# Kernel optimization log

Measured on AMD Instinct MI355X. Metric: run time of the kernel, lower is better.

## Reference

```python
import jax, jax.numpy as jnp
import numpy as np

EMBED_DIM = 1024
NUM_HEADS = 16
HEAD_DIM = EMBED_DIM // NUM_HEADS
SEQ_LEN = 2048
B = 2


def setup_inputs() -> dict:
    key = jax.random.key(0)
    ks = jax.random.split(key, 6)
    x = jax.random.normal(ks[0], (B, SEQ_LEN, EMBED_DIM), dtype=jnp.float32)
    # Linear params (torch Linear: y = x @ W.T + b); store W as [in, out] for einsum
    qkv_w = jax.random.normal(ks[1], (EMBED_DIM, 3 * EMBED_DIM), dtype=jnp.float32) * (EMBED_DIM ** -0.5)
    qkv_b = jnp.zeros((3 * EMBED_DIM,), dtype=jnp.float32)
    proj_w = jax.random.normal(ks[2], (EMBED_DIM, EMBED_DIM), dtype=jnp.float32) * (EMBED_DIM ** -0.5)
    proj_b = jnp.zeros((EMBED_DIM,), dtype=jnp.float32)
    # relative position bias table [2L-1, H], trunc_normal std=0.02 ~ normal*0.02
    bias_table = jax.random.normal(ks[3], (2 * SEQ_LEN - 1, NUM_HEADS), dtype=jnp.float32) * 0.02
    return {"x": x, "qkv_w": qkv_w, "qkv_b": qkv_b, "proj_w": proj_w, "proj_b": proj_b, "bias_table": bias_table}


def _rel_pos_index(L):
    coords = jnp.arange(L)
    return (coords[None, :] - coords[:, None]) + (SEQ_LEN - 1)  # [L, L] int


def reference(x, qkv_w, qkv_b, proj_w, proj_b, bias_table):
    Bsz, L, C = x.shape
    scale = HEAD_DIM ** -0.5
    qkv = x @ qkv_w + qkv_b                               # [B, L, 3C]
    qkv = qkv.reshape(Bsz, L, 3, NUM_HEADS, HEAD_DIM)
    q = jnp.transpose(qkv[:, :, 0], (0, 2, 1, 3))          # [B, H, L, D]
    k = jnp.transpose(qkv[:, :, 1], (0, 2, 1, 3))
    v = jnp.transpose(qkv[:, :, 2], (0, 2, 1, 3))
    attn = jnp.einsum('bhqd,bhkd->bhqk', q, k) * scale     # [B, H, L, L]
    rel_bias = bias_table[_rel_pos_index(L)]               # [L, L, H]
    attn = attn + jnp.transpose(rel_bias, (2, 0, 1))[None]  # broadcast over batch
    attn = jax.nn.softmax(attn, axis=-1)
    out = jnp.einsum('bhqk,bhkd->bhqd', attn, v)           # [B, H, L, D]
    out = jnp.transpose(out, (0, 2, 1, 3)).reshape(Bsz, L, C)
    return out @ proj_w + proj_b
```

## Files before the change

### kernel.cpp

```cpp
#include <hip/hip_runtime.h>

typedef short bf16x4 __attribute__((ext_vector_type(4)));
typedef short bf16x8 __attribute__((ext_vector_type(8)));
typedef float f32x4 __attribute__((ext_vector_type(4)));
typedef float f32x16 __attribute__((ext_vector_type(16)));

__device__ __forceinline__ unsigned short f2bf(float f) {
  union { float f; unsigned int u; } v; v.f = f;
  unsigned int r = v.u + 0x7FFFu + ((v.u >> 16) & 1u);
  return (unsigned short)(r >> 16);
}

__device__ __forceinline__ float exp2_fast(float x) {
  float r;
  asm("v_exp_f32 %0, %1" : "=v"(r) : "v"(x));
  return r;
}

__device__ __forceinline__ unsigned int cvt_pk_bf16(float lo, float hi) {
  unsigned int r;
  asm("v_cvt_pk_bf16_f32 %0, %1, %2" : "=v"(r) : "v"(lo), "v"(hi));
  return r;
}

__device__ __forceinline__ void gld_lds16(const void* g, void* l) {
  __builtin_amdgcn_global_load_lds(
      (const __attribute__((address_space(1))) unsigned int*)g,
      (__attribute__((address_space(3))) unsigned int*)l, 16, 0, 0);
}


__global__ __launch_bounds__(256) void k_convert_x(const float4* __restrict__ in,
                                                   ushort4* __restrict__ out) {
  int id = blockIdx.x * 256 + threadIdx.x;
  float4 v = in[id];
  ushort4 o;
  o.x = f2bf(v.x); o.y = f2bf(v.y); o.z = f2bf(v.z); o.w = f2bf(v.w);
  out[id] = o;
}

__global__ __launch_bounds__(256) void k_transpose_bf16(const float* __restrict__ in,
                                                        unsigned short* __restrict__ out,
                                                        int R, int C) {
  __shared__ float tile[32][33];
  int tx = threadIdx.x, ty = threadIdx.y;
  int c0 = blockIdx.x * 32, r0 = blockIdx.y * 32;
#pragma unroll
  for (int i = 0; i < 32; i += 8) tile[ty + i][tx] = in[(size_t)(r0 + ty + i) * C + c0 + tx];
  __syncthreads();
#pragma unroll
  for (int i = 0; i < 32; i += 8) out[(size_t)(c0 + ty + i) * R + r0 + tx] = f2bf(tile[tx][ty + i]);
}

__global__ __launch_bounds__(256) void k_bias_cols(const float* __restrict__ bt,
                                                   float* __restrict__ bh) {
  int i = blockIdx.x * 256 + threadIdx.x;
  if (i < 4095 * 16) bh[(i & 15) * 4096 + (i >> 4)] = bt[i] * 1.44269504089f;
}

template <int EPI>
__global__ __launch_bounds__(256) void k_gemm(const unsigned short* __restrict__ A,
                                              const unsigned short* __restrict__ Bt,
                                              const float* __restrict__ bias,
                                              float* __restrict__ Cf,
                                              unsigned short* __restrict__ qb,
                                              unsigned short* __restrict__ kb,
                                              unsigned short* __restrict__ vtb) {
  __shared__ unsigned short Alds[128 * 64];
  __shared__ unsigned short Blds[128 * 64];
  const int t = threadIdx.x;
  const int l = t & 63, w = t >> 6;
  const int l15 = l & 15, l4 = l >> 4;
  const int wm = w >> 1, wn = w & 1;

  constexpr int NX = EPI ? 24 : 8;
  constexpr int NWG = EPI ? 768 : 256;
  const int hwid = blockIdx.x + NX * blockIdx.y;
  const int swz = (hwid & 7) * (NWG >> 3) + (hwid >> 3);
  const int bn = (swz % NX) * 128;
  const int bm = (swz / NX) * 128;

  const int srow = t >> 3;
  const int scl = (t & 7) ^ (srow & 7);
  const unsigned short* ag = A + (size_t)(bm + srow) * 1024 + scl * 8;
  const unsigned short* bg = Bt + (size_t)(bn + srow) * 1024 + scl * 8;

  f32x4 acc[4][4];
#pragma unroll
  for (int i = 0; i < 4; ++i)
#pragma unroll
    for (int j = 0; j < 4; ++j) acc[i][j] = (f32x4){0.f, 0.f, 0.f, 0.f};

  for (int kt = 0; kt < 16; ++kt) {
#pragma unroll
    for (int q = 0; q < 4; ++q) {
      gld_lds16(ag + (size_t)q * 32 * 1024 + kt * 64, &Alds[(q * 256 + t) * 8]);
      gld_lds16(bg + (size_t)q * 32 * 1024 + kt * 64, &Blds[(q * 256 + t) * 8]);
    }
    __syncthreads();
#pragma unroll
    for (int kc = 0; kc < 2; ++kc) {
      bf16x8 af[4], bv[4];
#pragma unroll
      for (int i = 0; i < 4; ++i) {
        int ra = wm * 64 + i * 16 + l15;
        af[i] = *(const bf16x8*)&Alds[ra * 64 + (((kc * 4 + l4) ^ (l15 & 7))) * 8];
        int rb = wn * 64 + i * 16 + l15;
        bv[i] = *(const bf16x8*)&Blds[rb * 64 + (((kc * 4 + l4) ^ (l15 & 7))) * 8];
      }
#pragma unroll
      for (int i = 0; i < 4; ++i)
#pragma unroll
        for (int jn = 0; jn < 4; ++jn)
          acc[i][jn] = __builtin_amdgcn_mfma_f32_16x16x32_bf16(af[i], bv[jn], acc[i][jn], 0, 0, 0);
    }
    __syncthreads();
  }

#pragma unroll
  for (int i = 0; i < 4; ++i) {
#pragma unroll
    for (int jn = 0; jn < 4; ++jn) {
      int n = bn + wn * 64 + jn * 16 + l15;
      float bval = bias[n];
#pragma unroll
      for (int j = 0; j < 4; ++j) {
        int m = bm + wm * 64 + i * 16 + l4 * 4 + j;
        float v = acc[i][jn][j] + bval;
        if (EPI == 0) {
          Cf[(size_t)m * 1024 + n] = v;
        } else {
          int which = n >> 10, hh = (n >> 6) & 15, d = n & 63;
          int bb = m >> 11, pos = m & 2047;
          int bhh = bb * 16 + hh;
          if (which == 0)
            qb[((size_t)bhh * 2048 + pos) * 64 + d] = f2bf(v * 0.18033688f);
          else if (which == 1)
            kb[((size_t)bhh * 2048 + pos) * 64 + d] = f2bf(v);
          else
            vtb[((size_t)bhh * 64 + d) * 2048 + pos] = f2bf(v);
        }
      }
    }
  }
}

__global__ __launch_bounds__(256) void k_attn(const unsigned short* __restrict__ qbuf,
                                              const unsigned short* __restrict__ kbuf,
                                              const unsigned short* __restrict__ vtbuf,
                                              const float* __restrict__ biash,
                                              unsigned short* __restrict__ aout) {
  __shared__ __align__(16) unsigned short Klds[2][64 * 64];
  __shared__ __align__(16) unsigned short Vlds[2][64 * 64];

  const int t = threadIdx.x;
  const int w = t >> 6, l = t & 63;
  const int l31 = l & 31, hi = l >> 5;

  const int bid = blockIdx.x;
  const int swzb = (bid & 7) * 64 + (bid >> 3);
  const int qt = swzb & 15;
  const int bh = swzb >> 4;
  const int h = bh & 15, b = bh >> 4;
  const int qbase = qt * 128;
  const int wq = qbase + w * 32;

  bf16x8 qB[4];
  {
    const unsigned short* qrow = qbuf + ((size_t)bh * 2048 + wq + l31) * 64;
#pragma unroll
    for (int ds = 0; ds < 4; ++ds) qB[ds] = *(const bf16x8*)&qrow[ds * 16 + hi * 8];
  }

  f32x16 O[2];
#pragma unroll
  for (int i = 0; i < 16; ++i) { O[0][i] = 0.f; O[1][i] = 0.f; }
  float m_run = -3e38f, l_run = 0.f;

  const int c0r = t >> 3, c0c = t & 7;
  const unsigned short* kg = kbuf + ((size_t)bh * 2048 + c0r) * 64 + c0c * 8;
  const unsigned short* vg = vtbuf + ((size_t)bh * 64 + c0r) * 2048 + c0c * 8;
  const int wKV = c0r * 64 + ((c0c ^ (c0r & 7)) * 8);

  {
    bf16x8 k0 = *(const bf16x8*)(kg);
    bf16x8 k1 = *(const bf16x8*)(kg + 32 * 64);
    bf16x8 v0 = *(const bf16x8*)(vg);
    bf16x8 v1 = *(const bf16x8*)(vg + 32 * 2048);
    *(bf16x8*)&Klds[0][wKV] = k0;
    *(bf16x8*)&Klds[0][wKV + 2048] = k1;
    *(bf16x8*)&Vlds[0][wKV] = v0;
    *(bf16x8*)&Vlds[0][wKV + 2048] = v1;
  }
  __syncthreads();

  const float* bgl = biash + h * 4096 + 2047 - (wq + l31) + 4 * hi;

  for (int kt = 0; kt < 32; ++kt) {
    const int cur = kt & 1;

    bf16x8 kst0, kst1, vst0, vst1;
    if (kt < 31) {
      const unsigned short* kga = kg + (size_t)(kt + 1) * 4096;
      const unsigned short* vga = vg + (kt + 1) * 64;
      kst0 = *(const bf16x8*)(kga);
      kst1 = *(const bf16x8*)(kga + 32 * 64);
      vst0 = *(const bf16x8*)(vga);
      vst1 = *(const bf16x8*)(vga + 32 * 2048);
    }
    const int kbase = kt * 64;

    f32x4 bq[2][4];
#pragma unroll
    for (int kt2 = 0; kt2 < 2; ++kt2)
#pragma unroll
      for (int g = 0; g < 4; ++g)
        __builtin_memcpy(&bq[kt2][g], &bgl[kbase + 32 * kt2 + 8 * g], 16);

    f32x16 sacc[2];
#pragma unroll
    for (int i = 0; i < 16; ++i) { sacc[0][i] = 0.f; sacc[1][i] = 0.f; }
    __builtin_amdgcn_s_setprio(1);
#pragma unroll
    for (int kt2 = 0; kt2 < 2; ++kt2) {
      int row = kt2 * 32 + l31;
      int rsw = row & 7;
#pragma unroll
      for (int ds = 0; ds < 4; ++ds) {
        bf16x8 ka = *(const bf16x8*)&Klds[cur][row * 64 + (((2 * ds + hi) ^ rsw) * 8)];
        sacc[kt2] = __builtin_amdgcn_mfma_f32_32x32x16_bf16(ka, qB[ds], sacc[kt2], 0, 0, 0);
      }
    }
    __builtin_amdgcn_s_setprio(0);

#pragma unroll
    for (int kt2 = 0; kt2 < 2; ++kt2)
#pragma unroll
      for (int g = 0; g < 4; ++g)
#pragma unroll
        for (int r = 0; r < 4; ++r) sacc[kt2][4 * g + r] += bq[kt2][g][r];

    float mx;
    {
      float q0 = fmaxf(fmaxf(sacc[0][0], sacc[0][1]), fmaxf(sacc[0][2], sacc[0][3]));
      float q1 = fmaxf(fmaxf(sacc[0][4], sacc[0][5]), fmaxf(sacc[0][6], sacc[0][7]));
      float q2 = fmaxf(fmaxf(sacc[0][8], sacc[0][9]), fmaxf(sacc[0][10], sacc[0][11]));
      float q3 = fmaxf(fmaxf(sacc[0][12], sacc[0][13]), fmaxf(sacc[0][14], sacc[0][15]));
      float q4 = fmaxf(fmaxf(sacc[1][0], sacc[1][1]), fmaxf(sacc[1][2], sacc[1][3]));
      float q5 = fmaxf(fmaxf(sacc[1][4], sacc[1][5]), fmaxf(sacc[1][6], sacc[1][7]));
      float q6 = fmaxf(fmaxf(sacc[1][8], sacc[1][9]), fmaxf(sacc[1][10], sacc[1][11]));
      float q7 = fmaxf(fmaxf(sacc[1][12], sacc[1][13]), fmaxf(sacc[1][14], sacc[1][15]));
      mx = fmaxf(fmaxf(fmaxf(q0, q1), fmaxf(q2, q3)), fmaxf(fmaxf(q4, q5), fmaxf(q6, q7)));
      mx = fmaxf(mx, __shfl_xor(mx, 32));
    }

    if (__any(mx > m_run + 8.f)) {
      float mnew = fmaxf(m_run, mx);
      float alpha = exp2_fast(m_run - mnew);
      m_run = mnew;
      l_run *= alpha;
#pragma unroll
      for (int g = 0; g < 4; ++g)
#pragma unroll
        for (int r = 0; r < 4; ++r) {
          float a_lo = __shfl(alpha, 8 * g + r);
          float a_hi = __shfl(alpha, 8 * g + r + 4);
          float aq = hi ? a_hi : a_lo;
          O[0][4 * g + r] *= aq;
          O[1][4 * g + r] *= aq;
        }
    }

#pragma unroll
    for (int kt2 = 0; kt2 < 2; ++kt2)
#pragma unroll
      for (int i = 0; i < 16; ++i) sacc[kt2][i] = exp2_fast(sacc[kt2][i] - m_run);
    {
      float s0 = (sacc[0][0] + sacc[0][1]) + (sacc[0][2] + sacc[0][3]);
      float s1 = (sacc[0][4] + sacc[0][5]) + (sacc[0][6] + sacc[0][7]);
      float s2 = (sacc[0][8] + sacc[0][9]) + (sacc[0][10] + sacc[0][11]);
      float s3 = (sacc[0][12] + sacc[0][13]) + (sacc[0][14] + sacc[0][15]);
      float s4 = (sacc[1][0] + sacc[1][1]) + (sacc[1][2] + sacc[1][3]);
      float s5 = (sacc[1][4] + sacc[1][5]) + (sacc[1][6] + sacc[1][7]);
      float s6 = (sacc[1][8] + sacc[1][9]) + (sacc[1][10] + sacc[1][11]);
      float s7 = (sacc[1][12] + sacc[1][13]) + (sacc[1][14] + sacc[1][15]);
      float rs = ((s0 + s1) + (s2 + s3)) + ((s4 + s5) + (s6 + s7));
      rs += __shfl_xor(rs, 32);
      l_run += rs;
    }

    bf16x8 pa[2][2];
#pragma unroll
    for (int kt2 = 0; kt2 < 2; ++kt2)
#pragma unroll
      for (int mm = 0; mm < 2; ++mm) {
        union { unsigned int u[4]; bf16x8 v; } pk;
        pk.u[0] = cvt_pk_bf16(sacc[kt2][8 * mm + 0], sacc[kt2][8 * mm + 1]);
        pk.u[1] = cvt_pk_bf16(sacc[kt2][8 * mm + 2], sacc[kt2][8 * mm + 3]);
        pk.u[2] = cvt_pk_bf16(sacc[kt2][8 * mm + 4], sacc[kt2][8 * mm + 5]);
        pk.u[3] = cvt_pk_bf16(sacc[kt2][8 * mm + 6], sacc[kt2][8 * mm + 7]);
        pa[kt2][mm] = pk.v;
      }

    __builtin_amdgcn_s_setprio(1);
#pragma unroll
    for (int dt = 0; dt < 2; ++dt) {
      int row = dt * 32 + l31;
      int rsw = row & 7;
#pragma unroll
      for (int kt2 = 0; kt2 < 2; ++kt2)
#pragma unroll
        for (int mm = 0; mm < 2; ++mm) {
          int cA = (4 * kt2 + 2 * mm) ^ rsw;
          int cB = (4 * kt2 + 2 * mm + 1) ^ rsw;
          bf16x4 vlo = *(const bf16x4*)&Vlds[cur][row * 64 + cA * 8 + 4 * hi];
          bf16x4 vhi = *(const bf16x4*)&Vlds[cur][row * 64 + cB * 8 + 4 * hi];
          bf16x8 vb = __builtin_shufflevector(vlo, vhi, 0, 1, 2, 3, 4, 5, 6, 7);
          O[dt] = __builtin_amdgcn_mfma_f32_32x32x16_bf16(pa[kt2][mm], vb, O[dt], 0, 0, 0);
        }
    }
    __builtin_amdgcn_s_setprio(0);

    if (kt < 31) {
      *(bf16x8*)&Klds[cur ^ 1][wKV] = kst0;
      *(bf16x8*)&Klds[cur ^ 1][wKV + 2048] = kst1;
      *(bf16x8*)&Vlds[cur ^ 1][wKV] = vst0;
      *(bf16x8*)&Vlds[cur ^ 1][wKV + 2048] = vst1;
    }
    __syncthreads();
  }

  {
    float linv = 1.f / l_run;
#pragma unroll
    for (int g = 0; g < 4; ++g)
#pragma unroll
      for (int r = 0; r < 4; ++r) {
        float v_lo = __shfl(linv, 8 * g + r);
        float v_hi = __shfl(linv, 8 * g + r + 4);
        float sc = hi ? v_hi : v_lo;
        int q = wq + 8 * g + r + 4 * hi;
        size_t base = ((size_t)b * 2048 + q) * 1024 + h * 64 + l31;
        aout[base] = f2bf(O[0][4 * g + r] * sc);
        aout[base + 32] = f2bf(O[1][4 * g + r] * sc);
      }
  }
}


extern "C" void kernel_launch(void* const* d_in, const int* in_sizes, int n_in,
                              void* d_out, int out_size, void* d_ws, size_t ws_size,
                              hipStream_t stream) {
  const float* x = (const float*)d_in[0];
  const float* qkv_w = (const float*)d_in[1];
  const float* qkv_b = (const float*)d_in[2];
  const float* proj_w = (const float*)d_in[3];
  const float* proj_b = (const float*)d_in[4];
  const float* bias_table = (const float*)d_in[5];
  float* out = (float*)d_out;

  char* ws = (char*)d_ws;
  unsigned short* xb = (unsigned short*)(ws);
  unsigned short* wqkv = (unsigned short*)(ws + (size_t)(8u << 20));
  unsigned short* wproj = (unsigned short*)(ws + (size_t)(14u << 20));
  unsigned short* qb = (unsigned short*)(ws + (size_t)(16u << 20));
  unsigned short* kb = (unsigned short*)(ws + (size_t)(24u << 20));
  unsigned short* vtb = (unsigned short*)(ws + (size_t)(32u << 20));
  float* biash = (float*)(ws + (size_t)(40u << 20));

  unsigned short* attn_out = xb;

  k_convert_x<<<dim3(4096), dim3(256), 0, stream>>>((const float4*)x, (ushort4*)xb);
  k_transpose_bf16<<<dim3(96, 32), dim3(32, 8), 0, stream>>>(qkv_w, wqkv, 1024, 3072);
  k_transpose_bf16<<<dim3(32, 32), dim3(32, 8), 0, stream>>>(proj_w, wproj, 1024, 1024);
  k_bias_cols<<<dim3(256), dim3(256), 0, stream>>>(bias_table, biash);

  k_gemm<1><<<dim3(24, 32), dim3(256), 0, stream>>>(xb, wqkv, qkv_b, nullptr, qb, kb, vtb);
  k_attn<<<dim3(512), dim3(256), 0, stream>>>(qb, kb, vtb, biash, attn_out);
  k_gemm<0><<<dim3(8, 32), dim3(256), 0, stream>>>(attn_out, wproj, proj_b, out, nullptr, nullptr,
                                                   nullptr);
}
```

Before: 161.9 us.

## Double-buffer GEMM LDS with register-staged prefetch and XCD-aware tile mapping

The GEMM main loop moves from direct global-to-LDS loads with two barriers per k-step to a two-stage pipeline. Global loads for step k+2 go into registers while MFMAs run on the current LDS buffer, and the staged registers are written to the other LDS buffer, leaving one barrier per step. The block-to-tile mapping also changes to a 1D grid that groups each XCD's blocks into an 8x(12 or 4) tile region to improve L2 reuse. This costs double the LDS (64KB per block) and 16 extra VGPR vectors, which may lower occupancy.

```diff
diff --git a/kernel.cpp b/kernel.cpp
--- a/kernel.cpp
+++ b/kernel.cpp
@@ -21,12 +21,6 @@
   unsigned int r;
   asm("v_cvt_pk_bf16_f32 %0, %1, %2" : "=v"(r) : "v"(lo), "v"(hi));
   return r;
-}
-
-__device__ __forceinline__ void gld_lds16(const void* g, void* l) {
-  __builtin_amdgcn_global_load_lds(
-      (const __attribute__((address_space(1))) unsigned int*)g,
-      (__attribute__((address_space(3))) unsigned int*)l, 16, 0, 0);
 }
 
 
@@ -66,24 +60,23 @@
                                               unsigned short* __restrict__ qb,
                                               unsigned short* __restrict__ kb,
                                               unsigned short* __restrict__ vtb) {
-  __shared__ unsigned short Alds[128 * 64];
-  __shared__ unsigned short Blds[128 * 64];
+  __shared__ unsigned short Alds[2][128 * 64];
+  __shared__ unsigned short Blds[2][128 * 64];
   const int t = threadIdx.x;
   const int l = t & 63, w = t >> 6;
   const int l15 = l & 15, l4 = l >> 4;
   const int wm = w >> 1, wn = w & 1;
 
-  constexpr int NX = EPI ? 24 : 8;
-  constexpr int NWG = EPI ? 768 : 256;
-  const int hwid = blockIdx.x + NX * blockIdx.y;
-  const int swz = (hwid & 7) * (NWG >> 3) + (hwid >> 3);
-  const int bn = (swz % NX) * 128;
-  const int bm = (swz / NX) * 128;
+  const int hwid = blockIdx.x;
+  const int x = hwid & 7, loc = hwid >> 3;
+  const int bm = ((x >> 1) * 8 + (loc & 7)) * 128;
+  const int bn = ((x & 1) * (EPI ? 12 : 4) + (loc >> 3)) * 128;
 
   const int srow = t >> 3;
-  const int scl = (t & 7) ^ (srow & 7);
-  const unsigned short* ag = A + (size_t)(bm + srow) * 1024 + scl * 8;
-  const unsigned short* bg = Bt + (size_t)(bn + srow) * 1024 + scl * 8;
+  const int sc = t & 7;
+  const unsigned short* agl = A + (size_t)(bm + srow) * 1024 + sc * 8;
+  const unsigned short* bgl = Bt + (size_t)(bn + srow) * 1024 + sc * 8;
+  const int wls = srow * 64 + ((sc ^ (srow & 7)) * 8);
 
   f32x4 acc[4][4];
 #pragma unroll
@@ -91,31 +84,59 @@
 #pragma unroll
     for (int j = 0; j < 4; ++j) acc[i][j] = (f32x4){0.f, 0.f, 0.f, 0.f};
 
-  for (int kt = 0; kt < 16; ++kt) {
-#pragma unroll
-    for (int q = 0; q < 4; ++q) {
-      gld_lds16(ag + (size_t)q * 32 * 1024 + kt * 64, &Alds[(q * 256 + t) * 8]);
-      gld_lds16(bg + (size_t)q * 32 * 1024 + kt * 64, &Blds[(q * 256 + t) * 8]);
-    }
-    __syncthreads();
-#pragma unroll
-    for (int kc = 0; kc < 2; ++kc) {
-      bf16x8 af[4], bv[4];
-#pragma unroll
-      for (int i = 0; i < 4; ++i) {
-        int ra = wm * 64 + i * 16 + l15;
-        af[i] = *(const bf16x8*)&Alds[ra * 64 + (((kc * 4 + l4) ^ (l15 & 7))) * 8];
-        int rb = wn * 64 + i * 16 + l15;
-        bv[i] = *(const bf16x8*)&Blds[rb * 64 + (((kc * 4 + l4) ^ (l15 & 7))) * 8];
-      }
-#pragma unroll
-      for (int i = 0; i < 4; ++i)
-#pragma unroll
-        for (int jn = 0; jn < 4; ++jn)
-          acc[i][jn] = __builtin_amdgcn_mfma_f32_16x16x32_bf16(af[i], bv[jn], acc[i][jn], 0, 0, 0);
-    }
-    __syncthreads();
-  }
+  bf16x8 ra[8], rb[8];
+
+#define GLOAD(REGS, KT)                                                       \
+  _Pragma("unroll") for (int q = 0; q < 4; ++q) {                             \
+    REGS[q] = *(const bf16x8*)(agl + (size_t)q * 32768 + (KT) * 64);          \
+    REGS[4 + q] = *(const bf16x8*)(bgl + (size_t)q * 32768 + (KT) * 64);      \
+  }
+#define SWRITE(REGS, CUR)                                                     \
+  _Pragma("unroll") for (int q = 0; q < 4; ++q) {                             \
+    *(bf16x8*)&Alds[CUR][q * 2048 + wls] = REGS[q];                           \
+    *(bf16x8*)&Blds[CUR][q * 2048 + wls] = REGS[4 + q];                       \
+  }
+
+  GLOAD(ra, 0);
+  GLOAD(rb, 1);
+  SWRITE(ra, 0);
+  asm volatile("s_waitcnt lgkmcnt(0)" ::: "memory");
+  __builtin_amdgcn_s_barrier();
+
+#define GEMM_PHASE(KT, RFREE, RPEND)                                          \
+  {                                                                           \
+    const int cur_ = (KT) & 1;                                                \
+    if ((KT) + 2 < 16) { GLOAD(RFREE, (KT) + 2); }                            \
+    __builtin_amdgcn_s_setprio(1);                                            \
+    _Pragma("unroll") for (int kc = 0; kc < 2; ++kc) {                        \
+      bf16x8 af[4], bv[4];                                                    \
+      _Pragma("unroll") for (int i = 0; i < 4; ++i) {                         \
+        int ra_ = wm * 64 + i * 16 + l15;                                     \
+        af[i] = *(const bf16x8*)&Alds[cur_][ra_ * 64 +                        \
+                                            (((kc * 4 + l4) ^ (l15 & 7))) * 8]; \
+        int rb_ = wn * 64 + i * 16 + l15;                                     \
+        bv[i] = *(const bf16x8*)&Blds[cur_][rb_ * 64 +                        \
+                                            (((kc * 4 + l4) ^ (l15 & 7))) * 8]; \
+      }                                                                       \
+      _Pragma("unroll") for (int i = 0; i < 4; ++i)                           \
+        _Pragma("unroll") for (int jn = 0; jn < 4; ++jn)                      \
+          acc[i][jn] =                                                        \
+              __builtin_amdgcn_mfma_f32_16x16x32_bf16(af[i], bv[jn],          \
+                                                      acc[i][jn], 0, 0, 0);   \
+    }                                                                         \
+    __builtin_amdgcn_s_setprio(0);                                            \
+    if ((KT) + 1 < 16) { SWRITE(RPEND, cur_ ^ 1); }                           \
+    asm volatile("s_waitcnt lgkmcnt(0)" ::: "memory");                        \
+    __builtin_amdgcn_s_barrier();                                             \
+  }
+
+  for (int kt = 0; kt < 16; kt += 2) {
+    GEMM_PHASE(kt, ra, rb);
+    GEMM_PHASE(kt + 1, rb, ra);
+  }
+#undef GEMM_PHASE
+#undef SWRITE
+#undef GLOAD
 
 #pragma unroll
   for (int i = 0; i < 4; ++i) {
@@ -375,8 +396,8 @@
   k_transpose_bf16<<<dim3(32, 32), dim3(32, 8), 0, stream>>>(proj_w, wproj, 1024, 1024);
   k_bias_cols<<<dim3(256), dim3(256), 0, stream>>>(bias_table, biash);
 
-  k_gemm<1><<<dim3(24, 32), dim3(256), 0, stream>>>(xb, wqkv, qkv_b, nullptr, qb, kb, vtb);
+  k_gemm<1><<<dim3(768), dim3(256), 0, stream>>>(xb, wqkv, qkv_b, nullptr, qb, kb, vtb);
   k_attn<<<dim3(512), dim3(256), 0, stream>>>(qb, kb, vtb, biash, attn_out);
-  k_gemm<0><<<dim3(8, 32), dim3(256), 0, stream>>>(attn_out, wproj, proj_b, out, nullptr, nullptr,
-                                                   nullptr);
-}
+  k_gemm<0><<<dim3(256), dim3(256), 0, stream>>>(attn_out, wproj, proj_b, out, nullptr, nullptr,
+                                                 nullptr);
+}
```

Measured after the change: 156.7 us. 3.2% less time.
